# Kernel optimization log

Measured on AMD Instinct MI355X. Metric: run time of the kernel, lower is better.

Reference implementation:

```python
import jax, jax.numpy as jnp
import numpy as np


def setup_inputs() -> dict:
    key = jax.random.key(0)
    ks = jax.random.split(key, 6)
    B, L, NC = 32, 10000, 80
    REG_MAX, K, HID = 32, 4, 64
    IN = 4 * (K + 1)  # 20
    scores = jax.random.normal(ks[0], (B, L, NC), dtype=jnp.float32)
    pred_corners = jax.random.normal(ks[1], (B, L, 4 * (REG_MAX + 1)), dtype=jnp.float32)
    w1 = jax.random.normal(ks[2], (HID, IN), dtype=jnp.float32) * (1.0 / np.sqrt(IN))
    b1 = jax.random.normal(ks[3], (HID,), dtype=jnp.float32) * 0.01
    w2 = jax.random.normal(ks[4], (1, HID), dtype=jnp.float32) * (1.0 / np.sqrt(HID))
    b2 = jax.random.normal(ks[5], (1,), dtype=jnp.float32) * 0.01
    return {"scores": scores, "pred_corners": pred_corners,
            "w1": w1, "b1": b1, "w2": w2, "b2": b2, "k_top": K}


def reference(scores, pred_corners, w1, b1, w2, b2, k_top):
    B, L, D = pred_corners.shape
    nbins = D // 4  # reg_max + 1
    # softmax over the distribution bins of each of the 4 box sides
    prob = jax.nn.softmax(pred_corners.reshape(B, L, 4, nbins), axis=-1)
    prob_topk, _ = jax.lax.top_k(prob, k_top)                      # [B, L, 4, k]
    stat = jnp.concatenate(
        [prob_topk, prob_topk.mean(axis=-1, keepdims=True)], axis=-1)  # [B, L, 4, k+1]
    stat = stat.reshape(B, L, 4 * (k_top + 1))                     # [B, L, 4*(k+1)]
    # tiny MLP: Linear -> ReLU -> Linear
    h = jax.nn.relu(jnp.einsum('bli,hi->blh', stat, w1) + b1)      # [B, L, hid]
    quality = jnp.einsum('blh,oh->blo', h, w2) + b2                # [B, L, 1]
    return scores + quality
```

## Files before the change

### kernel.cpp

```cpp
#include <hip/hip_runtime.h>
#include <cstdint>
#include <cmath>


constexpr int NB   = 33;
constexpr int DPR  = 132;
constexpr int F4PA = 33;
constexpr int HID  = 64;
constexpr int NCLS = 80;
constexpr int APT  = 64;
constexpr int TPB  = 5;

__global__ __attribute__((amdgpu_flat_work_group_size(64, 64)))
void lqe_q(
    const float* __restrict__ pred,
    const float* __restrict__ w1,
    const float* __restrict__ b1,
    const float* __restrict__ w2,
    const float* __restrict__ b2,
    float* __restrict__ qout)
{
    __shared__ float4 s_buf[APT * F4PA];
    __shared__ float  s_w1[HID * 16];
    __shared__ float  s_b1[HID];
    __shared__ float  s_w2[HID];

    const int t = threadIdx.x;

    {
        float wr[20];
        const float4* ws = (const float4*)(w1 + t * 20);
        #pragma unroll
        for (int i = 0; i < 5; ++i) ((float4*)wr)[i] = ws[i];
        #pragma unroll
        for (int s = 0; s < 4; ++s) {
            float wm = 0.25f * wr[s * 5 + 4];
            #pragma unroll
            for (int q = 0; q < 4; ++q)
                s_w1[t * 16 + s * 4 + q] = wr[s * 5 + q] + wm;
        }
        s_b1[t] = b1[t];
        s_w2[t] = w2[t];
    }
    const float b2r = b2[0];
    __syncthreads();

    const long long tile0 = (long long)blockIdx.x * TPB;

    for (int i = 0; i < TPB; ++i) {
        const long long tile = tile0 + i;
        const float4* g4 = (const float4*)pred + tile * (APT * F4PA);

        #pragma unroll
        for (int g = 0; g < 4; ++g) {
            float4 r[8];
            #pragma unroll
            for (int j = 0; j < 8; ++j) r[j] = g4[(g * 8 + j) * 64 + t];
            #pragma unroll
            for (int j = 0; j < 8; ++j) s_buf[(g * 8 + j) * 64 + t] = r[j];
        }
        { float4 r = g4[32 * 64 + t]; s_buf[32 * 64 + t] = r; }

        __syncthreads();

        const float4* lp = (const float4*)s_buf + t * F4PA;
        float f[16];
        float e0 = 0.f, e1 = 0.f, e2 = 0.f, e3 = 0.f, sum = 0.f;
        #pragma unroll
        for (int ld = 0; ld < 33; ++ld) {
            float4 v4 = lp[ld];
            float vv[4] = {v4.x, v4.y, v4.z, v4.w};
            #pragma unroll
            for (int c = 0; c < 4; ++c) {
                const int idx = 4 * ld + c;
                float e = __expf(vv[c]);
                sum += e;
                float n0 = fminf(e0, e);  e0 = fmaxf(e0, e);
                float n1 = fminf(e1, n0); e1 = fmaxf(e1, n0);
                float n2 = fminf(e2, n1); e2 = fmaxf(e2, n1);
                e3 = fmaxf(e3, n2);
                if (idx % NB == NB - 1) {
                    const int s = idx / NB;
                    float inv = 1.0f / sum;
                    f[s * 4 + 0] = e0 * inv;
                    f[s * 4 + 1] = e1 * inv;
                    f[s * 4 + 2] = e2 * inv;
                    f[s * 4 + 3] = e3 * inv;
                    e0 = e1 = e2 = e3 = 0.f; sum = 0.f;
                }
            }
        }

        float qv = b2r;
        #pragma unroll
        for (int j = 0; j < HID; ++j) {
            const float4* wr = (const float4*)(s_w1 + j * 16);
            float hj = s_b1[j];
            #pragma unroll
            for (int i4 = 0; i4 < 4; ++i4) {
                float4 w = wr[i4];
                hj = fmaf(f[4 * i4 + 0], w.x, hj);
                hj = fmaf(f[4 * i4 + 1], w.y, hj);
                hj = fmaf(f[4 * i4 + 2], w.z, hj);
                hj = fmaf(f[4 * i4 + 3], w.w, hj);
            }
            hj = fmaxf(hj, 0.f);
            qv = fmaf(hj, s_w2[j], qv);
        }
        qout[tile * APT + t] = qv;

        __syncthreads();
    }
}

__global__ __launch_bounds__(256)
void lqe_add(
    const float* __restrict__ scores,
    const float* __restrict__ qin,
    float* __restrict__ out)
{
    const int i = blockIdx.x * 256 + threadIdx.x;
    const float q = qin[i / 20];
    float4 v = ((const float4*)scores)[i];
    v.x += q; v.y += q; v.z += q; v.w += q;
    ((float4*)out)[i] = v;
}

extern "C" void kernel_launch(void* const* d_in, const int* in_sizes, int n_in,
                              void* d_out, int out_size, void* d_ws, size_t ws_size,
                              hipStream_t stream) {
    const float* scores = (const float*)d_in[0];
    const float* pred   = (const float*)d_in[1];
    const float* w1     = (const float*)d_in[2];
    const float* b1     = (const float*)d_in[3];
    const float* w2     = (const float*)d_in[4];
    const float* b2     = (const float*)d_in[5];

    int n_anchor = in_sizes[0] / NCLS;
    float* qbuf  = (float*)d_ws;

    lqe_q<<<n_anchor / (APT * TPB), APT, 0, stream>>>(pred, w1, b1, w2, b2, qbuf);

    int nf4 = n_anchor * (NCLS / 4);
    lqe_add<<<nf4 / 256, 256, 0, stream>>>(scores, qbuf, (float*)d_out);
}
```

Baseline: 351.9 us.

## Split q kernel into two independent waves per block, batch add kernel per anchor group

```diff
diff --git a/kernel.cpp b/kernel.cpp
--- a/kernel.cpp
+++ b/kernel.cpp
@@ -4,14 +4,12 @@
 
 
 constexpr int NB   = 33;
-constexpr int DPR  = 132;
 constexpr int F4PA = 33;
 constexpr int HID  = 64;
 constexpr int NCLS = 80;
 constexpr int APT  = 64;
-constexpr int TPB  = 5;
 
-__global__ __attribute__((amdgpu_flat_work_group_size(64, 64)))
+__global__ __attribute__((amdgpu_flat_work_group_size(128, 128)))
 void lqe_q(
     const float* __restrict__ pred,
     const float* __restrict__ w1,
@@ -20,14 +18,14 @@
     const float* __restrict__ b2,
     float* __restrict__ qout)
 {
-    __shared__ float4 s_buf[APT * F4PA];
+    __shared__ float4 s_buf[2][APT * F4PA];
     __shared__ float  s_w1[HID * 16];
     __shared__ float  s_b1[HID];
     __shared__ float  s_w2[HID];
 
     const int t = threadIdx.x;
 
-    {
+    if (t < HID) {
         float wr[20];
         const float4* ws = (const float4*)(w1 + t * 20);
         #pragma unroll
@@ -45,72 +43,70 @@
     const float b2r = b2[0];
     __syncthreads();
 
-    const long long tile0 = (long long)blockIdx.x * TPB;
+    const int w = t >> 6;
+    const int l = t & 63;
+    const long long tile = (long long)blockIdx.x * 2 + w;
+    const float4* g4 = (const float4*)pred + tile * (APT * F4PA);
+    float4* sb = &s_buf[w][0];
 
-    for (int i = 0; i < TPB; ++i) {
-        const long long tile = tile0 + i;
-        const float4* g4 = (const float4*)pred + tile * (APT * F4PA);
+    #pragma unroll
+    for (int g = 0; g < 4; ++g) {
+        float4 r[8];
+        #pragma unroll
+        for (int j = 0; j < 8; ++j) r[j] = g4[(g * 8 + j) * 64 + l];
+        #pragma unroll
+        for (int j = 0; j < 8; ++j) sb[(g * 8 + j) * 64 + l] = r[j];
+    }
+    { float4 r = g4[32 * 64 + l]; sb[32 * 64 + l] = r; }
 
+    asm volatile("s_waitcnt lgkmcnt(0)" ::: "memory");
+    __builtin_amdgcn_sched_barrier(0);
+
+    const float4* lp = sb + l * F4PA;
+    float f[16];
+    float e0 = 0.f, e1 = 0.f, e2 = 0.f, e3 = 0.f, sum = 0.f;
+    #pragma unroll
+    for (int ld = 0; ld < 33; ++ld) {
+        float4 v4 = lp[ld];
+        float vv[4] = {v4.x, v4.y, v4.z, v4.w};
         #pragma unroll
-        for (int g = 0; g < 4; ++g) {
-            float4 r[8];
-            #pragma unroll
-            for (int j = 0; j < 8; ++j) r[j] = g4[(g * 8 + j) * 64 + t];
-            #pragma unroll
-            for (int j = 0; j < 8; ++j) s_buf[(g * 8 + j) * 64 + t] = r[j];
-        }
-        { float4 r = g4[32 * 64 + t]; s_buf[32 * 64 + t] = r; }
-
-        __syncthreads();
-
-        const float4* lp = (const float4*)s_buf + t * F4PA;
-        float f[16];
-        float e0 = 0.f, e1 = 0.f, e2 = 0.f, e3 = 0.f, sum = 0.f;
-        #pragma unroll
-        for (int ld = 0; ld < 33; ++ld) {
-            float4 v4 = lp[ld];
-            float vv[4] = {v4.x, v4.y, v4.z, v4.w};
-            #pragma unroll
-            for (int c = 0; c < 4; ++c) {
-                const int idx = 4 * ld + c;
-                float e = __expf(vv[c]);
-                sum += e;
-                float n0 = fminf(e0, e);  e0 = fmaxf(e0, e);
-                float n1 = fminf(e1, n0); e1 = fmaxf(e1, n0);
-                float n2 = fminf(e2, n1); e2 = fmaxf(e2, n1);
-                e3 = fmaxf(e3, n2);
-                if (idx % NB == NB - 1) {
-                    const int s = idx / NB;
-                    float inv = 1.0f / sum;
-                    f[s * 4 + 0] = e0 * inv;
-                    f[s * 4 + 1] = e1 * inv;
-                    f[s * 4 + 2] = e2 * inv;
-                    f[s * 4 + 3] = e3 * inv;
-                    e0 = e1 = e2 = e3 = 0.f; sum = 0.f;
-                }
+        for (int c = 0; c < 4; ++c) {
+            const int idx = 4 * ld + c;
+            float e = __expf(vv[c]);
+            sum += e;
+            float n0 = fminf(e0, e);  e0 = fmaxf(e0, e);
+            float n1 = fminf(e1, n0); e1 = fmaxf(e1, n0);
+            float n2 = fminf(e2, n1); e2 = fmaxf(e2, n1);
+            e3 = fmaxf(e3, n2);
+            if (idx % NB == NB - 1) {
+                const int s = idx / NB;
+                float inv = 1.0f / sum;
+                f[s * 4 + 0] = e0 * inv;
+                f[s * 4 + 1] = e1 * inv;
+                f[s * 4 + 2] = e2 * inv;
+                f[s * 4 + 3] = e3 * inv;
+                e0 = e1 = e2 = e3 = 0.f; sum = 0.f;
             }
         }
+    }
 
-        float qv = b2r;
+    float qv = b2r;
+    #pragma unroll
+    for (int j = 0; j < HID; ++j) {
+        const float4* wr = (const float4*)(s_w1 + j * 16);
+        float hj = s_b1[j];
         #pragma unroll
-        for (int j = 0; j < HID; ++j) {
-            const float4* wr = (const float4*)(s_w1 + j * 16);
-            float hj = s_b1[j];
-            #pragma unroll
-            for (int i4 = 0; i4 < 4; ++i4) {
-                float4 w = wr[i4];
-                hj = fmaf(f[4 * i4 + 0], w.x, hj);
-                hj = fmaf(f[4 * i4 + 1], w.y, hj);
-                hj = fmaf(f[4 * i4 + 2], w.z, hj);
-                hj = fmaf(f[4 * i4 + 3], w.w, hj);
-            }
-            hj = fmaxf(hj, 0.f);
-            qv = fmaf(hj, s_w2[j], qv);
+        for (int i4 = 0; i4 < 4; ++i4) {
+            float4 wv = wr[i4];
+            hj = fmaf(f[4 * i4 + 0], wv.x, hj);
+            hj = fmaf(f[4 * i4 + 1], wv.y, hj);
+            hj = fmaf(f[4 * i4 + 2], wv.z, hj);
+            hj = fmaf(f[4 * i4 + 3], wv.w, hj);
         }
-        qout[tile * APT + t] = qv;
-
-        __syncthreads();
+        hj = fmaxf(hj, 0.f);
+        qv = fmaf(hj, s_w2[j], qv);
     }
+    qout[tile * APT + l] = qv;
 }
 
 __global__ __launch_bounds__(256)
@@ -119,11 +115,32 @@
     const float* __restrict__ qin,
     float* __restrict__ out)
 {
-    const int i = blockIdx.x * 256 + threadIdx.x;
-    const float q = qin[i / 20];
-    float4 v = ((const float4*)scores)[i];
-    v.x += q; v.y += q; v.z += q; v.w += q;
-    ((float4*)out)[i] = v;
+    __shared__ float s_q[64];
+    const int t = threadIdx.x;
+    const long long a0 = (long long)blockIdx.x * 64;
+
+    if (t < 64) s_q[t] = qin[a0 + t];
+    __syncthreads();
+
+    const float4* sc4 = (const float4*)(scores + a0 * NCLS);
+    float4*       ot4 = (float4*)(out + a0 * NCLS);
+
+    float4 v[5];
+    float  q[5];
+    #pragma unroll
+    for (int u = 0; u < 5; ++u) {
+        const int i = u * 256 + t;
+        v[u] = sc4[i];
+        q[u] = s_q[i / 20];
+    }
+    #pragma unroll
+    for (int u = 0; u < 5; ++u) {
+        const int i = u * 256 + t;
+        float4 x = v[u];
+        float qq = q[u];
+        x.x += qq; x.y += qq; x.z += qq; x.w += qq;
+        ot4[i] = x;
+    }
 }
 
 extern "C" void kernel_launch(void* const* d_in, const int* in_sizes, int n_in,
@@ -139,8 +156,7 @@
     int n_anchor = in_sizes[0] / NCLS;
     float* qbuf  = (float*)d_ws;
 
-    lqe_q<<<n_anchor / (APT * TPB), APT, 0, stream>>>(pred, w1, b1, w2, b2, qbuf);
+    lqe_q<<<n_anchor / 128, 128, 0, stream>>>(pred, w1, b1, w2, b2, qbuf);
 
-    int nf4 = n_anchor * (NCLS / 4);
-    lqe_add<<<nf4 / 256, 256, 0, stream>>>(scores, qbuf, (float*)d_out);
+    lqe_add<<<n_anchor / 64, 256, 0, stream>>>(scores, qbuf, (float*)d_out);
 }
```

New measurement: 366.6 us. 1.04x slower.
